# Performance work log

Measured on AMD Instinct MI355X. Metric: run time of the kernel, lower is better.

Reference implementation:

```python
import jax, jax.numpy as jnp
import numpy as np

D_MODEL, N_HEADS = 1024, 16
HEAD_DIM = D_MODEL // N_HEADS  # 64
BS, Q_LEN, SEQ_LEN = 4, 1024, 1024


def setup_inputs() -> dict:
    key = jax.random.key(0)
    kq, kk, kv, kp, km = jax.random.split(key, 5)
    q = jax.random.normal(kq, (BS, N_HEADS, Q_LEN, HEAD_DIM), dtype=jnp.float32)
    k = jax.random.normal(kk, (BS, N_HEADS, HEAD_DIM, SEQ_LEN), dtype=jnp.float32)
    v = jax.random.normal(kv, (BS, N_HEADS, SEQ_LEN, HEAD_DIM), dtype=jnp.float32)
    prev = jax.random.normal(kp, (BS, N_HEADS, Q_LEN, SEQ_LEN), dtype=jnp.float32)
    attn_weighted_mask = jax.random.uniform(km, (1, N_HEADS, Q_LEN, SEQ_LEN), dtype=jnp.float32)
    scale = jnp.asarray(HEAD_DIM ** (-0.5), dtype=jnp.float32)  # nn.Parameter scalar
    return {"q": q, "k": k, "v": v, "prev": prev,
            "attn_weighted_mask": attn_weighted_mask, "scale": scale}


def reference(q, k, v, prev, attn_weighted_mask, scale):
    # scores = (q @ k) * scale + prev       [bs, h, q_len, seq_len]
    attn_scores = jnp.einsum('bhqd,bhds->bhqs', q, k) * scale + prev
    # softmax over keys; attn_dropout p=0.0 -> identity
    attn_weights = jax.nn.softmax(attn_scores, axis=-1)
    # post-softmax elementwise weighted mask
    attn_weights = attn_weights * attn_weighted_mask
    # output = attn_weights @ v             [bs, h, q_len, d_v]
    output = jnp.einsum('bhqs,bhsd->bhqd', attn_weights, v)
    # res_attention=True -> also return weights and pre-softmax scores
    return output, attn_weights, attn_scores
```

## Files before the change

kernel.cpp:

```cpp
#include <hip/hip_runtime.h>


#define QL 1024
#define SL 1024
#define HD 64

typedef __attribute__((ext_vector_type(8))) short bf16x8;
typedef __attribute__((ext_vector_type(4))) short bf16x4;
typedef __attribute__((ext_vector_type(4))) float f32x4;

__device__ __forceinline__ short f2bf(float f) {
    union { float f; unsigned u; } v; v.f = f;
    unsigned r = v.u + 0x7FFFu + ((v.u >> 16) & 1u);
    return (short)(r >> 16);
}

__global__ __launch_bounds__(256) void _prepack_kv(
    const float* __restrict__ k, const float* __restrict__ v,
    short* __restrict__ ws)
{
    __shared__ short tile[64][72];
    const int t = threadIdx.x;
    int b = blockIdx.x;
    const float* src; short* dst; int ld_src, ld_dst;
    if (b < 1024) {
        const int bh = b >> 4, st = b & 15;
        src = k + (size_t)bh * 65536 + st * 64;               ld_src = 1024;
        dst = ws + (size_t)bh * 65536 + (size_t)st * 4096;    ld_dst = 64;
    } else {
        b -= 1024;
        const int bh = b >> 4, st = b & 15;
        src = v + (size_t)bh * 65536 + (size_t)st * 4096;     ld_src = 64;
        dst = ws + 4194304 + (size_t)bh * 65536 + st * 64;    ld_dst = 1024;
    }
    {
        const int r = t >> 2, c0 = (t & 3) * 16;
#pragma unroll
        for (int i = 0; i < 4; ++i) {
            float4 f = *(const float4*)&src[(size_t)r * ld_src + c0 + 4 * i];
            bf16x4 s4 = { f2bf(f.x), f2bf(f.y), f2bf(f.z), f2bf(f.w) };
            *(bf16x4*)&tile[r][c0 + 4 * i] = s4;
        }
    }
    __syncthreads();
    {
        const int r = t >> 2, c0 = (t & 3) * 16;
        bf16x8 o0, o1;
#pragma unroll
        for (int j = 0; j < 8; ++j) o0[j] = tile[c0 + j][r];
#pragma unroll
        for (int j = 0; j < 8; ++j) o1[j] = tile[c0 + 8 + j][r];
        *(bf16x8*)&dst[(size_t)r * ld_dst + c0]     = o0;
        *(bf16x8*)&dst[(size_t)r * ld_dst + c0 + 8] = o1;
    }
}

__global__ __launch_bounds__(512, 8) void _attn_main(
    const float* __restrict__ q, const float* __restrict__ prev,
    const float* __restrict__ mask, const float* __restrict__ scale_p,
    const short* __restrict__ Kt, const short* __restrict__ Vt,
    float* __restrict__ out)
{
    __shared__ short wbuf[16384];
    __shared__ float red[128];
    __shared__ float obuf[1024];

    const int tid  = threadIdx.x;
    const int w    = tid >> 6;
    const int lane = tid & 63;
    const int quad = lane >> 4;
    const int lp   = lane & 15;

    const int blk = (blockIdx.x & 7) * 512 + (blockIdx.x >> 3);
    const int bh  = blk >> 6;
    const int qt  = blk & 63;
    const int h   = bh & 15;
    const int q0  = qt * 16;

    const float scale = scale_p[0];

    const float* Qb = q    + (size_t)bh * QL * HD + (size_t)q0 * HD;
    const float* Pb = prev + (size_t)bh * QL * SL + (size_t)q0 * SL;
    const float* Mb = mask + (size_t)h  * QL * SL + (size_t)q0 * SL;
    const short* Kb = Kt + (size_t)bh * (SL * HD);
    const short* Vb = Vt + (size_t)bh * (SL * HD);

    float* Ob   = out            + (size_t)bh * QL * HD + (size_t)q0 * HD;
    float* Wout = out + 4194304  + (size_t)bh * QL * SL + (size_t)q0 * SL;
    float* Sout = out + 71303168 + (size_t)bh * QL * SL + (size_t)q0 * SL;

    const int s0 = 128 * w;

    f32x4 acc[8];
#pragma unroll
    for (int t = 0; t < 8; ++t) {
#pragma unroll
        for (int r = 0; r < 4; ++r)
            acc[t][r] = Pb[(size_t)(quad * 4 + r) * SL + s0 + 16 * t + lp];
    }

    bf16x8 aq[2];
#pragma unroll
    for (int ks = 0; ks < 2; ++ks) {
        const float* qp = Qb + (size_t)lp * HD + ks * 32 + quad * 8;
        float4 a = *(const float4*)qp;
        float4 b = *(const float4*)(qp + 4);
        aq[ks][0] = f2bf(a.x * scale); aq[ks][1] = f2bf(a.y * scale);
        aq[ks][2] = f2bf(a.z * scale); aq[ks][3] = f2bf(a.w * scale);
        aq[ks][4] = f2bf(b.x * scale); aq[ks][5] = f2bf(b.y * scale);
        aq[ks][6] = f2bf(b.z * scale); aq[ks][7] = f2bf(b.w * scale);
    }

#pragma unroll
    for (int ks = 0; ks < 2; ++ks) {
#pragma unroll
        for (int t = 0; t < 8; ++t) {
            bf16x8 bk = *(const bf16x8*)&Kb[(size_t)(s0 + 16 * t + lp) * HD
                                            + ks * 32 + quad * 8];
            acc[t] = __builtin_amdgcn_mfma_f32_16x16x32_bf16(aq[ks], bk, acc[t], 0, 0, 0);
        }
    }

    float lsum[4] = {0.f, 0.f, 0.f, 0.f};
#pragma unroll
    for (int t = 0; t < 8; ++t) {
#pragma unroll
        for (int r = 0; r < 4; ++r) {
            const int row = quad * 4 + r;
            const int col = s0 + 16 * t + lp;
            float sv = acc[t][r];
            Sout[(size_t)row * SL + col] = sv;
            float e = __expf(sv);
            acc[t][r] = e;
            lsum[r] += e;
        }
    }
#pragma unroll
    for (int r = 0; r < 4; ++r) {
        float s = lsum[r];
        s += __shfl_xor(s, 1);  s += __shfl_xor(s, 2);
        s += __shfl_xor(s, 4);  s += __shfl_xor(s, 8);
        lsum[r] = s;
    }
    if (lp == 0) {
#pragma unroll
        for (int r = 0; r < 4; ++r) red[w * 16 + quad * 4 + r] = lsum[r];
    }
    __syncthreads();
    float rinv[4];
#pragma unroll
    for (int r = 0; r < 4; ++r) {
        float s = 0.f;
#pragma unroll
        for (int u = 0; u < 8; ++u) s += red[u * 16 + quad * 4 + r];
        rinv[r] = 1.0f / s;
    }

#pragma unroll
    for (int t = 0; t < 8; ++t) {
#pragma unroll
        for (int r = 0; r < 4; ++r) {
            const int row = quad * 4 + r;
            const int col = s0 + 16 * t + lp;
            float wv = acc[t][r] * rinv[r] * Mb[(size_t)row * SL + col];
            Wout[(size_t)row * SL + col] = wv;
            wbuf[(((col >> 3) * 16) + row) * 8 + (lp & 7)] = f2bf(wv);
        }
    }
    __syncthreads();

    const int dgrp = w & 3;
    const int kh   = w >> 2;
    f32x4 oacc = {0.f, 0.f, 0.f, 0.f};
#pragma unroll 8
    for (int kk = 0; kk < 16; ++kk) {
        const int ks = kh * 16 + kk;
        bf16x8 aw = *(const bf16x8*)&wbuf[((ks * 4 + quad) * 16 + lp) * 8];
        bf16x8 bv = *(const bf16x8*)&Vb[(size_t)(16 * dgrp + lp) * SL
                                        + ks * 32 + quad * 8];
        oacc = __builtin_amdgcn_mfma_f32_16x16x32_bf16(aw, bv, oacc, 0, 0, 0);
    }
    if (kh == 1) {
#pragma unroll
        for (int r = 0; r < 4; ++r)
            obuf[(quad * 4 + r) * 64 + 16 * dgrp + lp] = oacc[r];
    }
    __syncthreads();
    if (kh == 0) {
#pragma unroll
        for (int r = 0; r < 4; ++r)
            Ob[(size_t)(quad * 4 + r) * HD + 16 * dgrp + lp]
                = oacc[r] + obuf[(quad * 4 + r) * 64 + 16 * dgrp + lp];
    }
}

__global__ __launch_bounds__(256) void _attn_fallback(
    const float* __restrict__ q, const float* __restrict__ k,
    const float* __restrict__ v, const float* __restrict__ prev,
    const float* __restrict__ mask, const float* __restrict__ scale_p,
    float* __restrict__ out)
{
    const int WSTR = SL + 8;
    __shared__ short wbuf[16 * (SL + 8)];
    __shared__ float red[4 * 16];

    const int tid  = threadIdx.x;
    const int w    = tid >> 6;
    const int lane = tid & 63;
    const int quad = lane >> 4;
    const int lp   = lane & 15;

    const int blk = blockIdx.x;
    const int bh  = blk >> 6;
    const int qt  = blk & 63;
    const int h   = bh & 15;
    const int q0  = qt * 16;

    const float scale = scale_p[0];

    const float* Qb = q    + (size_t)bh * QL * HD + (size_t)q0 * HD;
    const float* Kb = k    + (size_t)bh * HD * SL;
    const float* Vb = v    + (size_t)bh * SL * HD;
    const float* Pb = prev + (size_t)bh * QL * SL + (size_t)q0 * SL;
    const float* Mb = mask + (size_t)h  * QL * SL + (size_t)q0 * SL;

    float* Ob   = out            + (size_t)bh * QL * HD + (size_t)q0 * HD;
    float* Wout = out + 4194304  + (size_t)bh * QL * SL + (size_t)q0 * SL;
    float* Sout = out + 71303168 + (size_t)bh * QL * SL + (size_t)q0 * SL;

    bf16x8 aq[2];
#pragma unroll
    for (int ks = 0; ks < 2; ++ks) {
        const float* qp = Qb + (size_t)lp * HD + ks * 32 + quad * 8;
#pragma unroll
        for (int j = 0; j < 8; ++j) aq[ks][j] = f2bf(qp[j] * scale);
    }

    const int s0 = 256 * w;
    f32x4 acc[16];
#pragma unroll
    for (int t = 0; t < 16; ++t) {
#pragma unroll
        for (int r = 0; r < 4; ++r)
            acc[t][r] = Pb[(size_t)(quad * 4 + r) * SL + s0 + 16 * t + lp];
    }
#pragma unroll
    for (int ks = 0; ks < 2; ++ks) {
#pragma unroll
        for (int t = 0; t < 16; ++t) {
            bf16x8 bk;
            const float* kp = Kb + (size_t)(ks * 32 + quad * 8) * SL + s0 + 16 * t + lp;
#pragma unroll
            for (int j = 0; j < 8; ++j) bk[j] = f2bf(kp[(size_t)j * SL]);
            acc[t] = __builtin_amdgcn_mfma_f32_16x16x32_bf16(aq[ks], bk, acc[t], 0, 0, 0);
        }
    }

    float lsum[4] = {0.f, 0.f, 0.f, 0.f};
#pragma unroll
    for (int t = 0; t < 16; ++t) {
#pragma unroll
        for (int r = 0; r < 4; ++r) {
            float sv = acc[t][r];
            Sout[(size_t)(quad * 4 + r) * SL + s0 + 16 * t + lp] = sv;
            float e = __expf(sv);
            acc[t][r] = e;
            lsum[r] += e;
        }
    }
#pragma unroll
    for (int r = 0; r < 4; ++r) {
        float s = lsum[r];
        s += __shfl_xor(s, 1);  s += __shfl_xor(s, 2);
        s += __shfl_xor(s, 4);  s += __shfl_xor(s, 8);
        lsum[r] = s;
    }
    if (lp == 0) {
#pragma unroll
        for (int r = 0; r < 4; ++r) red[w * 16 + quad * 4 + r] = lsum[r];
    }
    __syncthreads();
    float rinv[4];
#pragma unroll
    for (int r = 0; r < 4; ++r) {
        float s = red[0 * 16 + quad * 4 + r] + red[1 * 16 + quad * 4 + r]
                + red[2 * 16 + quad * 4 + r] + red[3 * 16 + quad * 4 + r];
        rinv[r] = 1.0f / s;
    }

#pragma unroll
    for (int t = 0; t < 16; ++t) {
#pragma unroll
        for (int r = 0; r < 4; ++r) {
            int row = quad * 4 + r;
            int col = s0 + 16 * t + lp;
            float wv = acc[t][r] * rinv[r] * Mb[(size_t)row * SL + col];
            Wout[(size_t)row * SL + col] = wv;
            wbuf[row * WSTR + col] = f2bf(wv);
        }
    }
    __syncthreads();

    f32x4 oacc = {0.f, 0.f, 0.f, 0.f};
#pragma unroll 4
    for (int ks = 0; ks < 32; ++ks) {
        bf16x8 aw = *(const bf16x8*)&wbuf[lp * WSTR + ks * 32 + quad * 8];
        bf16x8 bv;
        const float* vp = Vb + (size_t)(ks * 32 + quad * 8) * HD + 16 * w + lp;
#pragma unroll
        for (int j = 0; j < 8; ++j) bv[j] = f2bf(vp[(size_t)j * HD]);
        oacc = __builtin_amdgcn_mfma_f32_16x16x32_bf16(aw, bv, oacc, 0, 0, 0);
    }
#pragma unroll
    for (int r = 0; r < 4; ++r)
        Ob[(size_t)(quad * 4 + r) * HD + 16 * w + lp] = oacc[r];
}

extern "C" void kernel_launch(void* const* d_in, const int* in_sizes, int n_in,
                              void* d_out, int out_size, void* d_ws, size_t ws_size,
                              hipStream_t stream) {
    const float* q     = (const float*)d_in[0];
    const float* k     = (const float*)d_in[1];
    const float* v     = (const float*)d_in[2];
    const float* prev  = (const float*)d_in[3];
    const float* mask  = (const float*)d_in[4];
    const float* scale = (const float*)d_in[5];
    float* out = (float*)d_out;

    if (d_ws != nullptr && ws_size >= (size_t)16 * 1024 * 1024) {
        short* ws = (short*)d_ws;
        _prepack_kv<<<dim3(2048), dim3(256), 0, stream>>>(k, v, ws);
        _attn_main<<<dim3(4096), dim3(512), 0, stream>>>(
            q, prev, mask, scale, ws, ws + 4194304, out);
    } else {
        _attn_fallback<<<dim3(4096), dim3(256), 0, stream>>>(
            q, k, v, prev, mask, scale, out);
    }
}
```

Measured before the change: 983.6 us.

## Swap MFMA operands to get row-contiguous accumulators and vectorize global IO

Swaps the A/B operands of both MFMAs so each lane's accumulator holds four consecutive columns of one query row instead of four rows of one column. This turns the prev, mask, scores, weights and output accesses into 16-byte vector loads and stores, and reduces the row-sum reduction to two shuffles. Mask loads are split into two batches, one before and one after the softmax sync, and the occupancy hint drops from 8 to 6 to make room for the extra registers. Per-lane rows are now 4KB apart, so each wave's coalescing pattern changes.

```diff
diff --git a/kernel.cpp b/kernel.cpp
--- a/kernel.cpp
+++ b/kernel.cpp
@@ -55,7 +55,7 @@
     }
 }
 
-__global__ __launch_bounds__(512, 8) void _attn_main(
+__global__ __launch_bounds__(512, 6) void _attn_main(
     const float* __restrict__ q, const float* __restrict__ prev,
     const float* __restrict__ mask, const float* __restrict__ scale_p,
     const short* __restrict__ Kt, const short* __restrict__ Vt,
@@ -90,13 +90,14 @@
     float* Sout = out + 71303168 + (size_t)bh * QL * SL + (size_t)q0 * SL;
 
     const int s0 = 128 * w;
+    const int sq = s0 + quad * 4;
 
     f32x4 acc[8];
-#pragma unroll
-    for (int t = 0; t < 8; ++t) {
-#pragma unroll
-        for (int r = 0; r < 4; ++r)
-            acc[t][r] = Pb[(size_t)(quad * 4 + r) * SL + s0 + 16 * t + lp];
+    {
+        const float* pp = Pb + (size_t)lp * SL + sq;
+#pragma unroll
+        for (int t = 0; t < 8; ++t)
+            acc[t] = *(const f32x4*)(pp + 16 * t);
     }
 
     bf16x8 aq[2];
@@ -117,54 +118,62 @@
         for (int t = 0; t < 8; ++t) {
             bf16x8 bk = *(const bf16x8*)&Kb[(size_t)(s0 + 16 * t + lp) * HD
                                             + ks * 32 + quad * 8];
-            acc[t] = __builtin_amdgcn_mfma_f32_16x16x32_bf16(aq[ks], bk, acc[t], 0, 0, 0);
-        }
-    }
-
-    float lsum[4] = {0.f, 0.f, 0.f, 0.f};
-#pragma unroll
-    for (int t = 0; t < 8; ++t) {
-#pragma unroll
-        for (int r = 0; r < 4; ++r) {
-            const int row = quad * 4 + r;
-            const int col = s0 + 16 * t + lp;
-            float sv = acc[t][r];
-            Sout[(size_t)row * SL + col] = sv;
-            float e = __expf(sv);
-            acc[t][r] = e;
-            lsum[r] += e;
-        }
-    }
-#pragma unroll
-    for (int r = 0; r < 4; ++r) {
-        float s = lsum[r];
-        s += __shfl_xor(s, 1);  s += __shfl_xor(s, 2);
-        s += __shfl_xor(s, 4);  s += __shfl_xor(s, 8);
-        lsum[r] = s;
-    }
-    if (lp == 0) {
-#pragma unroll
-        for (int r = 0; r < 4; ++r) red[w * 16 + quad * 4 + r] = lsum[r];
-    }
-    __syncthreads();
-    float rinv[4];
-#pragma unroll
-    for (int r = 0; r < 4; ++r) {
-        float s = 0.f;
-#pragma unroll
-        for (int u = 0; u < 8; ++u) s += red[u * 16 + quad * 4 + r];
-        rinv[r] = 1.0f / s;
-    }
-
-#pragma unroll
-    for (int t = 0; t < 8; ++t) {
-#pragma unroll
-        for (int r = 0; r < 4; ++r) {
-            const int row = quad * 4 + r;
-            const int col = s0 + 16 * t + lp;
-            float wv = acc[t][r] * rinv[r] * Mb[(size_t)row * SL + col];
-            Wout[(size_t)row * SL + col] = wv;
-            wbuf[(((col >> 3) * 16) + row) * 8 + (lp & 7)] = f2bf(wv);
+            acc[t] = __builtin_amdgcn_mfma_f32_16x16x32_bf16(bk, aq[ks], acc[t], 0, 0, 0);
+        }
+    }
+
+    float4 mkA[4];
+    {
+        const float* mp = Mb + (size_t)lp * SL + sq;
+#pragma unroll
+        for (int t = 0; t < 4; ++t)
+            mkA[t] = *(const float4*)(mp + 16 * t);
+    }
+
+    float lsum = 0.f;
+    {
+        float* sp = Sout + (size_t)lp * SL + sq;
+#pragma unroll
+        for (int t = 0; t < 8; ++t) {
+            f32x4 sv = acc[t];
+            *(f32x4*)(sp + 16 * t) = sv;
+#pragma unroll
+            for (int r = 0; r < 4; ++r) {
+                float e = __expf(sv[r]);
+                acc[t][r] = e;
+                lsum += e;
+            }
+        }
+    }
+    lsum += __shfl_xor(lsum, 16);
+    lsum += __shfl_xor(lsum, 32);
+    if (lane < 16) red[w * 16 + lane] = lsum;
+    __syncthreads();
+    float rsum = 0.f;
+#pragma unroll
+    for (int u = 0; u < 8; ++u) rsum += red[u * 16 + lp];
+    const float rinv = 1.0f / rsum;
+
+    float4 mkB[4];
+    {
+        const float* mp = Mb + (size_t)lp * SL + sq + 64;
+#pragma unroll
+        for (int t = 0; t < 4; ++t)
+            mkB[t] = *(const float4*)(mp + 16 * t);
+    }
+
+    {
+        float* wp = Wout + (size_t)lp * SL + sq;
+#pragma unroll
+        for (int t = 0; t < 8; ++t) {
+            float4 m4 = (t < 4) ? mkA[t] : mkB[t - 4];
+            f32x4 wv;
+#pragma unroll
+            for (int r = 0; r < 4; ++r) wv[r] = acc[t][r] * rinv * m4[r];
+            *(f32x4*)(wp + 16 * t) = wv;
+            const int sb = sq + 16 * t;
+            bf16x4 wb = { f2bf(wv[0]), f2bf(wv[1]), f2bf(wv[2]), f2bf(wv[3]) };
+            *(bf16x4*)&wbuf[((sb >> 3) * 16 + lp) * 8 + (sb & 4)] = wb;
         }
     }
     __syncthreads();
@@ -178,19 +187,17 @@
         bf16x8 aw = *(const bf16x8*)&wbuf[((ks * 4 + quad) * 16 + lp) * 8];
         bf16x8 bv = *(const bf16x8*)&Vb[(size_t)(16 * dgrp + lp) * SL
                                         + ks * 32 + quad * 8];
-        oacc = __builtin_amdgcn_mfma_f32_16x16x32_bf16(aw, bv, oacc, 0, 0, 0);
+        oacc = __builtin_amdgcn_mfma_f32_16x16x32_bf16(bv, aw, oacc, 0, 0, 0);
     }
     if (kh == 1) {
-#pragma unroll
-        for (int r = 0; r < 4; ++r)
-            obuf[(quad * 4 + r) * 64 + 16 * dgrp + lp] = oacc[r];
+        *(f32x4*)&obuf[lp * 64 + 16 * dgrp + quad * 4] = oacc;
     }
     __syncthreads();
     if (kh == 0) {
-#pragma unroll
-        for (int r = 0; r < 4; ++r)
-            Ob[(size_t)(quad * 4 + r) * HD + 16 * dgrp + lp]
-                = oacc[r] + obuf[(quad * 4 + r) * 64 + 16 * dgrp + lp];
+        f32x4 ov = *(const f32x4*)&obuf[lp * 64 + 16 * dgrp + quad * 4];
+#pragma unroll
+        for (int r = 0; r < 4; ++r) ov[r] += oacc[r];
+        *(f32x4*)&Ob[(size_t)lp * HD + 16 * dgrp + quad * 4] = ov;
     }
 }
 
```

Result: faster. 927.0 us (-5.8%).
